# Performance work log

Measured on AMD Instinct MI355X. Metric: run time of the kernel, lower is better.

The kernel has to match this reference:

```python
import jax, jax.numpy as jnp
import numpy as np

Lx, Ly, P, D, B = 6, 6, 2, 4, 8192


def _site(peps, i, j, s):
    # peps[i, j] : (P, up, down, left, right); select physical index s,
    # then slice open-boundary bonds down to width 1.
    t = peps[i, j][s]
    if i == 0:
        t = t[:1]
    if i == Lx - 1:
        t = t[:, :1]
    if j == 0:
        t = t[:, :, :1]
    if j == Ly - 1:
        t = t[:, :, :, :1]
    return t  # (u, d, l, r)


def _amp(xrow, peps):
    # Exact boundary contraction, sweeping columns left->right.
    # env axes: (l_0, ..., l_{Lx-1}) = left bonds of the current column.
    env = jnp.ones((1,) * Lx, dtype=peps.dtype)
    for j in range(Ly):
        env = env[None, ...]  # prepend u_0 (dim 1) for the top row
        for i in range(Lx):
            t = _site(peps, i, j, xrow[i * Ly + j])
            # contract vertical bond (axis i) and left bond (axis i+1)
            env = jnp.tensordot(env, t, axes=[[i, i + 1], [0, 2]])
            # new axes (d, r) appended at end -> move r to pos i, d to pos i+1
            env = jnp.moveaxis(env, (-1, -2), (i, i + 1))
        env = env[..., 0]  # bottom vertical bond has dim 1
    return env.reshape(())


def setup_inputs() -> dict:
    key = jax.random.key(0)
    kx, kp = jax.random.split(key)
    x = jax.random.randint(kx, (B, Lx * Ly), 0, P, dtype=jnp.int32)
    # scale 0.25 keeps the product of 36 random tensors O(1) (each tensordot
    # sums D^2=16 random products -> growth ~4*sigma per site)
    peps = 0.25 * jax.random.normal(kp, (Lx, Ly, P, D, D, D, D), dtype=jnp.float32)
    return {"x": x, "peps": peps}


def reference(x, peps):
    # batched amplitudes, one scalar per configuration
    return jax.vmap(_amp, in_axes=(0, None))(x, peps)
```

## Files before the change

kernel.cpp:

```cpp
#include <hip/hip_runtime.h>

#define LX 6
#define LY 6
#define NSITE 36
#define TSZ (NSITE * 2 * 256)

__device__ float g_Tt[TSZ];

__global__ __launch_bounds__(256) void build_T_kernel(const float* __restrict__ peps) {
    int idx = blockIdx.x * 256 + threadIdx.x;
    if (idx >= TSZ) return;
    int o    = idx & 15;
    int vl   = (idx >> 4) & 15;
    int s    = (idx >> 8) & 1;
    int site = idx >> 9;
    int i = site / LY, j = site - i * LY;
    int v = vl & 3, l = vl >> 2, vp = o & 3, rp = o >> 2;
    bool ok = (i > 0 || v == 0) && (i < LX - 1 || vp == 0) &&
              (j > 0 || l == 0) && (j < LY - 1 || rp == 0);
    g_Tt[idx] = ok ? peps[site * 512 + s * 256 + v * 64 + vp * 16 + l * 4 + rp] : 0.0f;
}

__device__ __forceinline__ int swz(int f) {
    return f ^ ((((f >> 5) ^ (f >> 8)) & 7) << 2);
}

__device__ __forceinline__ void fma4(float4& a, float s, const float4& t) {
    a.x = __builtin_fmaf(s, t.x, a.x);
    a.y = __builtin_fmaf(s, t.y, a.y);
    a.z = __builtin_fmaf(s, t.z, a.z);
    a.w = __builtin_fmaf(s, t.w, a.w);
}

__device__ __forceinline__ float f4c(const float4& v, int i) {
    return i == 0 ? v.x : i == 1 ? v.y : i == 2 ? v.z : v.w;
}

template<int I, bool TOPB, bool BOTB>
__device__ __forceinline__ void fused_pair(float* env, const float* __restrict__ T1,
                                           const float* __restrict__ T2, int tid) {
    constexpr int S1 = 1 << (2 * I + 2);
    constexpr int S2 = S1 << 2;
    const int lo = tid & ((1 << (2 * I)) - 1);
    const int hi = tid >> (2 * I);
    const int base = 4 * lo + (hi << (2 * I + 6));

    float4 inter[4][4];
    #pragma unroll
    for (int ap = 0; ap < 4; ++ap)
        #pragma unroll
        for (int bb = 0; bb < 4; ++bb)
            inter[ap][bb] = make_float4(0.f, 0.f, 0.f, 0.f);

    if (TOPB) {
        #pragma unroll
        for (int a = 0; a < 4; ++a) {
            float in0[4];
            #pragma unroll
            for (int bb = 0; bb < 4; ++bb)
                in0[bb] = env[swz(base + a * S1 + bb * S2)];
            #pragma unroll
            for (int ap = 0; ap < 4; ++ap) {
                float4 t1 = *(const float4*)(T1 + (4 * a) * 16 + 4 * ap);
                #pragma unroll
                for (int bb = 0; bb < 4; ++bb)
                    fma4(inter[ap][bb], in0[bb], t1);
            }
        }
    } else {
        #pragma unroll
        for (int a = 0; a < 4; ++a) {
            float4 inv[4];
            #pragma unroll
            for (int bb = 0; bb < 4; ++bb)
                inv[bb] = *(const float4*)&env[swz(base + a * S1 + bb * S2)];
            #pragma unroll
            for (int v = 0; v < 4; ++v) {
                #pragma unroll
                for (int ap = 0; ap < 4; ++ap) {
                    float4 t1 = *(const float4*)(T1 + (v + 4 * a) * 16 + 4 * ap);
                    #pragma unroll
                    for (int bb = 0; bb < 4; ++bb)
                        fma4(inter[ap][bb], f4c(inv[bb], v), t1);
                }
            }
        }
    }

    #pragma unroll
    for (int ap = 0; ap < 4; ++ap) {
        if (BOTB) {
            float o[4] = {0.f, 0.f, 0.f, 0.f};
            #pragma unroll
            for (int bb = 0; bb < 4; ++bb)
                #pragma unroll
                for (int vp = 0; vp < 4; ++vp) {
                    float iv = f4c(inter[ap][bb], vp);
                    #pragma unroll
                    for (int bp = 0; bp < 4; ++bp)
                        o[bp] = __builtin_fmaf(iv, T2[(vp + 4 * bb) * 16 + 4 * bp], o[bp]);
                }
            #pragma unroll
            for (int bp = 0; bp < 4; ++bp)
                *(float4*)&env[swz(base + ap * S1 + bp * S2)] = make_float4(o[bp], 0.f, 0.f, 0.f);
        } else {
            float4 outv[4];
            #pragma unroll
            for (int bp = 0; bp < 4; ++bp) outv[bp] = make_float4(0.f, 0.f, 0.f, 0.f);
            #pragma unroll
            for (int bb = 0; bb < 4; ++bb)
                #pragma unroll
                for (int vp = 0; vp < 4; ++vp) {
                    float iv = f4c(inter[ap][bb], vp);
                    #pragma unroll
                    for (int bp = 0; bp < 4; ++bp) {
                        float4 t2 = *(const float4*)(T2 + (vp + 4 * bb) * 16 + 4 * bp);
                        fma4(outv[bp], iv, t2);
                    }
                }
            #pragma unroll
            for (int bp = 0; bp < 4; ++bp)
                *(float4*)&env[swz(base + ap * S1 + bp * S2)] = outv[bp];
        }
    }
}

__global__ __launch_bounds__(256, 2) void peps_amp_kernel(const int* __restrict__ x,
                                                          float* __restrict__ out) {
    __shared__ float env[16384];
    const int tid = threadIdx.x;
    const int b = blockIdx.x;
    const int* xr = x + b * NSITE;

    #pragma unroll
    for (int p = 0; p < 16; ++p)
        *(float4*)&env[(tid + p * 256) * 4] = make_float4(0.f, 0.f, 0.f, 0.f);
    __syncthreads();

    {
        const float* A0 = g_Tt + ((0 * LY + 0) * 2 + __builtin_amdgcn_readfirstlane(xr[0 * LY])) * 256;
        const float* A1 = g_Tt + ((1 * LY + 0) * 2 + __builtin_amdgcn_readfirstlane(xr[1 * LY])) * 256;
        const float* A2 = g_Tt + ((2 * LY + 0) * 2 + __builtin_amdgcn_readfirstlane(xr[2 * LY])) * 256;
        const float* A3 = g_Tt + ((3 * LY + 0) * 2 + __builtin_amdgcn_readfirstlane(xr[3 * LY])) * 256;
        const float* A4 = g_Tt + ((4 * LY + 0) * 2 + __builtin_amdgcn_readfirstlane(xr[4 * LY])) * 256;
        const float* A5 = g_Tt + ((5 * LY + 0) * 2 + __builtin_amdgcn_readfirstlane(xr[5 * LY])) * 256;
        const int r2 = tid & 3, r3 = (tid >> 2) & 3, r4 = (tid >> 4) & 3, r5 = (tid >> 6) & 3;
        float w[4], w2[4];
        #pragma unroll
        for (int u = 0; u < 4; ++u) w[u] = A5[u * 16 + 4 * r5];
        #pragma unroll
        for (int u = 0; u < 4; ++u) { float acc = 0;
            #pragma unroll
            for (int d = 0; d < 4; ++d) acc = __builtin_fmaf(A4[u * 16 + d + 4 * r4], w[d], acc);
            w2[u] = acc; }
        #pragma unroll
        for (int u = 0; u < 4; ++u) { float acc = 0;
            #pragma unroll
            for (int d = 0; d < 4; ++d) acc = __builtin_fmaf(A3[u * 16 + d + 4 * r3], w2[d], acc);
            w[u] = acc; }
        #pragma unroll
        for (int u = 0; u < 4; ++u) { float acc = 0;
            #pragma unroll
            for (int d = 0; d < 4; ++d) acc = __builtin_fmaf(A2[u * 16 + d + 4 * r2], w[d], acc);
            w2[u] = acc; }
        #pragma unroll
        for (int r1 = 0; r1 < 4; ++r1) {
            float u1[4];
            #pragma unroll
            for (int u = 0; u < 4; ++u) { float acc = 0;
                #pragma unroll
                for (int d = 0; d < 4; ++d) acc = __builtin_fmaf(A1[u * 16 + d + 4 * r1], w2[d], acc);
                u1[u] = acc; }
            #pragma unroll
            for (int r0 = 0; r0 < 4; ++r0) {
                float acc = 0;
                #pragma unroll
                for (int d = 0; d < 4; ++d) acc = __builtin_fmaf(A0[d + 4 * r0], u1[d], acc);
                env[swz(4 * (r0 + 4 * r1 + 16 * tid))] = acc;
            }
        }
    }
    __syncthreads();

    #pragma unroll 1
    for (int j = 1; j < LY - 1; ++j) {
        const float* T0 = g_Tt + ((0 * LY + j) * 2 + __builtin_amdgcn_readfirstlane(xr[0 * LY + j])) * 256;
        const float* T1 = g_Tt + ((1 * LY + j) * 2 + __builtin_amdgcn_readfirstlane(xr[1 * LY + j])) * 256;
        const float* T2 = g_Tt + ((2 * LY + j) * 2 + __builtin_amdgcn_readfirstlane(xr[2 * LY + j])) * 256;
        const float* T3 = g_Tt + ((3 * LY + j) * 2 + __builtin_amdgcn_readfirstlane(xr[3 * LY + j])) * 256;
        const float* T4 = g_Tt + ((4 * LY + j) * 2 + __builtin_amdgcn_readfirstlane(xr[4 * LY + j])) * 256;
        const float* T5 = g_Tt + ((5 * LY + j) * 2 + __builtin_amdgcn_readfirstlane(xr[5 * LY + j])) * 256;
        fused_pair<0, true,  false>(env, T0, T1, tid); __syncthreads();
        fused_pair<2, false, false>(env, T2, T3, tid); __syncthreads();
        fused_pair<4, false, true >(env, T4, T5, tid); __syncthreads();
    }

    {
        const float* B0 = g_Tt + ((0 * LY + 5) * 2 + __builtin_amdgcn_readfirstlane(xr[0 * LY + 5])) * 256;
        const float* B1 = g_Tt + ((1 * LY + 5) * 2 + __builtin_amdgcn_readfirstlane(xr[1 * LY + 5])) * 256;
        const float* B2 = g_Tt + ((2 * LY + 5) * 2 + __builtin_amdgcn_readfirstlane(xr[2 * LY + 5])) * 256;
        const float* B3 = g_Tt + ((3 * LY + 5) * 2 + __builtin_amdgcn_readfirstlane(xr[3 * LY + 5])) * 256;
        const float* B4 = g_Tt + ((4 * LY + 5) * 2 + __builtin_amdgcn_readfirstlane(xr[4 * LY + 5])) * 256;
        const float* B5 = g_Tt + ((5 * LY + 5) * 2 + __builtin_amdgcn_readfirstlane(xr[5 * LY + 5])) * 256;
        const int l2 = tid & 3, l3 = (tid >> 2) & 3, l4 = (tid >> 4) & 3, l5 = (tid >> 6) & 3;
        float w[4], w2[4];
        #pragma unroll
        for (int u = 0; u < 4; ++u) w[u] = B5[(u + 4 * l5) * 16];
        #pragma unroll
        for (int u = 0; u < 4; ++u) { float acc = 0;
            #pragma unroll
            for (int d = 0; d < 4; ++d) acc = __builtin_fmaf(B4[(u + 4 * l4) * 16 + d], w[d], acc);
            w2[u] = acc; }
        #pragma unroll
        for (int u = 0; u < 4; ++u) { float acc = 0;
            #pragma unroll
            for (int d = 0; d < 4; ++d) acc = __builtin_fmaf(B3[(u + 4 * l3) * 16 + d], w2[d], acc);
            w[u] = acc; }
        #pragma unroll
        for (int u = 0; u < 4; ++u) { float acc = 0;
            #pragma unroll
            for (int d = 0; d < 4; ++d) acc = __builtin_fmaf(B2[(u + 4 * l2) * 16 + d], w[d], acc);
            w2[u] = acc; }
        float partial = 0.f;
        #pragma unroll
        for (int l1 = 0; l1 < 4; ++l1) {
            float u1[4];
            #pragma unroll
            for (int u = 0; u < 4; ++u) { float acc = 0;
                #pragma unroll
                for (int d = 0; d < 4; ++d) acc = __builtin_fmaf(B1[(u + 4 * l1) * 16 + d], w2[d], acc);
                u1[u] = acc; }
            #pragma unroll
            for (int l0 = 0; l0 < 4; ++l0) {
                float wv = 0.f;
                #pragma unroll
                for (int d = 0; d < 4; ++d) wv = __builtin_fmaf(B0[(4 * l0) * 16 + d], u1[d], wv);
                partial = __builtin_fmaf(env[swz(4 * (l0 + 4 * l1 + 16 * tid))], wv, partial);
            }
        }
        #pragma unroll
        for (int off = 32; off; off >>= 1) partial += __shfl_down(partial, off);
        __syncthreads();
        if ((tid & 63) == 0) env[tid >> 6] = partial;
        __syncthreads();
        if (tid == 0) out[b] = env[0] + env[1] + env[2] + env[3];
    }
}

extern "C" void kernel_launch(void* const* d_in, const int* in_sizes, int n_in,
                              void* d_out, int out_size, void* d_ws, size_t ws_size,
                              hipStream_t stream) {
    const int* x = (const int*)d_in[0];
    const float* peps = (const float*)d_in[1];
    float* out = (float*)d_out;

    build_T_kernel<<<(TSZ + 255) / 256, 256, 0, stream>>>(peps);
    peps_amp_kernel<<<out_size, 256, 0, stream>>>(x, out);
}
```

Before: 1.114 ms.

## Split each env tile across two threads with 512-thread blocks

Doubles the block to 512 threads. Each pair of threads now shares one env slice, and each thread computes half of the output ap/r1 indices, which halves per-thread register accumulators and FMA work. The shared-memory zero-initialisation pass is removed, since every entry read is written first, and the final reduction sums eight wave partials instead of four. The aim is more resident waves per CU to hide LDS and FMA latency, at the cost of duplicated env input loads per thread pair.

```diff
diff --git a/kernel.cpp b/kernel.cpp
--- a/kernel.cpp
+++ b/kernel.cpp
@@ -38,19 +38,20 @@
 
 template<int I, bool TOPB, bool BOTB>
 __device__ __forceinline__ void fused_pair(float* env, const float* __restrict__ T1,
-                                           const float* __restrict__ T2, int tid) {
+                                           const float* __restrict__ T2,
+                                           int rest, int apBase) {
     constexpr int S1 = 1 << (2 * I + 2);
     constexpr int S2 = S1 << 2;
-    const int lo = tid & ((1 << (2 * I)) - 1);
-    const int hi = tid >> (2 * I);
+    const int lo = rest & ((1 << (2 * I)) - 1);
+    const int hi = rest >> (2 * I);
     const int base = 4 * lo + (hi << (2 * I + 6));
 
-    float4 inter[4][4];
+    float4 inter[2][4];
     #pragma unroll
-    for (int ap = 0; ap < 4; ++ap)
+    for (int k = 0; k < 2; ++k)
         #pragma unroll
         for (int bb = 0; bb < 4; ++bb)
-            inter[ap][bb] = make_float4(0.f, 0.f, 0.f, 0.f);
+            inter[k][bb] = make_float4(0.f, 0.f, 0.f, 0.f);
 
     if (TOPB) {
         #pragma unroll
@@ -60,11 +61,11 @@
             for (int bb = 0; bb < 4; ++bb)
                 in0[bb] = env[swz(base + a * S1 + bb * S2)];
             #pragma unroll
-            for (int ap = 0; ap < 4; ++ap) {
-                float4 t1 = *(const float4*)(T1 + (4 * a) * 16 + 4 * ap);
+            for (int k = 0; k < 2; ++k) {
+                float4 t1 = *(const float4*)(T1 + (4 * a) * 16 + 4 * (apBase + k));
                 #pragma unroll
                 for (int bb = 0; bb < 4; ++bb)
-                    fma4(inter[ap][bb], in0[bb], t1);
+                    fma4(inter[k][bb], in0[bb], t1);
             }
         }
     } else {
@@ -75,27 +76,27 @@
             for (int bb = 0; bb < 4; ++bb)
                 inv[bb] = *(const float4*)&env[swz(base + a * S1 + bb * S2)];
             #pragma unroll
-            for (int v = 0; v < 4; ++v) {
-                #pragma unroll
-                for (int ap = 0; ap < 4; ++ap) {
-                    float4 t1 = *(const float4*)(T1 + (v + 4 * a) * 16 + 4 * ap);
+            for (int v = 0; v < 4; ++v)
+                #pragma unroll
+                for (int k = 0; k < 2; ++k) {
+                    float4 t1 = *(const float4*)(T1 + (v + 4 * a) * 16 + 4 * (apBase + k));
                     #pragma unroll
                     for (int bb = 0; bb < 4; ++bb)
-                        fma4(inter[ap][bb], f4c(inv[bb], v), t1);
+                        fma4(inter[k][bb], f4c(inv[bb], v), t1);
                 }
-            }
         }
     }
 
     #pragma unroll
-    for (int ap = 0; ap < 4; ++ap) {
+    for (int k = 0; k < 2; ++k) {
+        const int ap = apBase + k;
         if (BOTB) {
             float o[4] = {0.f, 0.f, 0.f, 0.f};
             #pragma unroll
             for (int bb = 0; bb < 4; ++bb)
                 #pragma unroll
                 for (int vp = 0; vp < 4; ++vp) {
-                    float iv = f4c(inter[ap][bb], vp);
+                    float iv = f4c(inter[k][bb], vp);
                     #pragma unroll
                     for (int bp = 0; bp < 4; ++bp)
                         o[bp] = __builtin_fmaf(iv, T2[(vp + 4 * bb) * 16 + 4 * bp], o[bp]);
@@ -111,7 +112,7 @@
             for (int bb = 0; bb < 4; ++bb)
                 #pragma unroll
                 for (int vp = 0; vp < 4; ++vp) {
-                    float iv = f4c(inter[ap][bb], vp);
+                    float iv = f4c(inter[k][bb], vp);
                     #pragma unroll
                     for (int bp = 0; bp < 4; ++bp) {
                         float4 t2 = *(const float4*)(T2 + (vp + 4 * bb) * 16 + 4 * bp);
@@ -125,17 +126,15 @@
     }
 }
 
-__global__ __launch_bounds__(256, 2) void peps_amp_kernel(const int* __restrict__ x,
+__global__ __launch_bounds__(512, 4) void peps_amp_kernel(const int* __restrict__ x,
                                                           float* __restrict__ out) {
     __shared__ float env[16384];
     const int tid = threadIdx.x;
     const int b = blockIdx.x;
     const int* xr = x + b * NSITE;
-
-    #pragma unroll
-    for (int p = 0; p < 16; ++p)
-        *(float4*)&env[(tid + p * 256) * 4] = make_float4(0.f, 0.f, 0.f, 0.f);
-    __syncthreads();
+    const int rest = tid >> 1;
+    const int apBase = (tid & 1) * 2;
+
 
     {
         const float* A0 = g_Tt + ((0 * LY + 0) * 2 + __builtin_amdgcn_readfirstlane(xr[0 * LY])) * 256;
@@ -144,7 +143,7 @@
         const float* A3 = g_Tt + ((3 * LY + 0) * 2 + __builtin_amdgcn_readfirstlane(xr[3 * LY])) * 256;
         const float* A4 = g_Tt + ((4 * LY + 0) * 2 + __builtin_amdgcn_readfirstlane(xr[4 * LY])) * 256;
         const float* A5 = g_Tt + ((5 * LY + 0) * 2 + __builtin_amdgcn_readfirstlane(xr[5 * LY])) * 256;
-        const int r2 = tid & 3, r3 = (tid >> 2) & 3, r4 = (tid >> 4) & 3, r5 = (tid >> 6) & 3;
+        const int r2 = rest & 3, r3 = (rest >> 2) & 3, r4 = (rest >> 4) & 3, r5 = (rest >> 6) & 3;
         float w[4], w2[4];
         #pragma unroll
         for (int u = 0; u < 4; ++u) w[u] = A5[u * 16 + 4 * r5];
@@ -164,7 +163,8 @@
             for (int d = 0; d < 4; ++d) acc = __builtin_fmaf(A2[u * 16 + d + 4 * r2], w[d], acc);
             w2[u] = acc; }
         #pragma unroll
-        for (int r1 = 0; r1 < 4; ++r1) {
+        for (int t = 0; t < 2; ++t) {
+            const int r1 = apBase + t;
             float u1[4];
             #pragma unroll
             for (int u = 0; u < 4; ++u) { float acc = 0;
@@ -176,7 +176,7 @@
                 float acc = 0;
                 #pragma unroll
                 for (int d = 0; d < 4; ++d) acc = __builtin_fmaf(A0[d + 4 * r0], u1[d], acc);
-                env[swz(4 * (r0 + 4 * r1 + 16 * tid))] = acc;
+                env[swz(4 * r0 + 16 * r1 + 64 * rest)] = acc;
             }
         }
     }
@@ -190,9 +190,9 @@
         const float* T3 = g_Tt + ((3 * LY + j) * 2 + __builtin_amdgcn_readfirstlane(xr[3 * LY + j])) * 256;
         const float* T4 = g_Tt + ((4 * LY + j) * 2 + __builtin_amdgcn_readfirstlane(xr[4 * LY + j])) * 256;
         const float* T5 = g_Tt + ((5 * LY + j) * 2 + __builtin_amdgcn_readfirstlane(xr[5 * LY + j])) * 256;
-        fused_pair<0, true,  false>(env, T0, T1, tid); __syncthreads();
-        fused_pair<2, false, false>(env, T2, T3, tid); __syncthreads();
-        fused_pair<4, false, true >(env, T4, T5, tid); __syncthreads();
+        fused_pair<0, true,  false>(env, T0, T1, rest, apBase); __syncthreads();
+        fused_pair<2, false, false>(env, T2, T3, rest, apBase); __syncthreads();
+        fused_pair<4, false, true >(env, T4, T5, rest, apBase); __syncthreads();
     }
 
     {
@@ -202,7 +202,7 @@
         const float* B3 = g_Tt + ((3 * LY + 5) * 2 + __builtin_amdgcn_readfirstlane(xr[3 * LY + 5])) * 256;
         const float* B4 = g_Tt + ((4 * LY + 5) * 2 + __builtin_amdgcn_readfirstlane(xr[4 * LY + 5])) * 256;
         const float* B5 = g_Tt + ((5 * LY + 5) * 2 + __builtin_amdgcn_readfirstlane(xr[5 * LY + 5])) * 256;
-        const int l2 = tid & 3, l3 = (tid >> 2) & 3, l4 = (tid >> 4) & 3, l5 = (tid >> 6) & 3;
+        const int l2 = rest & 3, l3 = (rest >> 2) & 3, l4 = (rest >> 4) & 3, l5 = (rest >> 6) & 3;
         float w[4], w2[4];
         #pragma unroll
         for (int u = 0; u < 4; ++u) w[u] = B5[(u + 4 * l5) * 16];
@@ -223,7 +223,8 @@
             w2[u] = acc; }
         float partial = 0.f;
         #pragma unroll
-        for (int l1 = 0; l1 < 4; ++l1) {
+        for (int t = 0; t < 2; ++t) {
+            const int l1 = apBase + t;
             float u1[4];
             #pragma unroll
             for (int u = 0; u < 4; ++u) { float acc = 0;
@@ -235,7 +236,7 @@
                 float wv = 0.f;
                 #pragma unroll
                 for (int d = 0; d < 4; ++d) wv = __builtin_fmaf(B0[(4 * l0) * 16 + d], u1[d], wv);
-                partial = __builtin_fmaf(env[swz(4 * (l0 + 4 * l1 + 16 * tid))], wv, partial);
+                partial = __builtin_fmaf(env[swz(4 * l0 + 16 * l1 + 64 * rest)], wv, partial);
             }
         }
         #pragma unroll
@@ -243,7 +244,9 @@
         __syncthreads();
         if ((tid & 63) == 0) env[tid >> 6] = partial;
         __syncthreads();
-        if (tid == 0) out[b] = env[0] + env[1] + env[2] + env[3];
+        if (tid == 0)
+            out[b] = ((env[0] + env[1]) + (env[2] + env[3]))
+                   + ((env[4] + env[5]) + (env[6] + env[7]));
     }
 }
 
@@ -255,5 +258,5 @@
     float* out = (float*)d_out;
 
     build_T_kernel<<<(TSZ + 255) / 256, 256, 0, stream>>>(peps);
-    peps_amp_kernel<<<out_size, 256, 0, stream>>>(x, out);
-}
+    peps_amp_kernel<<<out_size, 512, 0, stream>>>(x, out);
+}
```

New measurement: 1.536 ms. +37.9%, slower.
